# Kernel tuning notes

Hardware: AMD Instinct MI355X
Metric: run time of the kernel (lower is better)

Reference implementation:

```python
import jax, jax.numpy as jnp
import numpy as np

BLOCK = 64
# NF4 codebook (normal-float 4-bit values, as in QLoRA/torchao)
NF4_TABLE = jnp.array([
    -1.0, -0.6961928009986877, -0.5250730514526367, -0.39491748809814453,
    -0.28444138169288635, -0.18477343022823334, -0.09105003625154495, 0.0,
    0.07958029955625534, 0.16093020141124725, 0.24611230194568634,
    0.33791524171829224, 0.44070982933044434, 0.5626170039176941,
    0.7229568362236023, 1.0], dtype=jnp.float32)

D_MODEL, HIDDEN = 4096, 11008
BATCH, SEQ = 2, 2048


def setup_inputs() -> dict:
    key = jax.random.key(0)
    ks = jax.random.split(key, 7)
    x = jax.random.normal(ks[0], (BATCH, SEQ, D_MODEL), dtype=jnp.float32)
    w1_q = jax.random.randint(ks[1], (HIDDEN, D_MODEL), 0, 16, dtype=jnp.int32)
    w2_q = jax.random.randint(ks[2], (HIDDEN, D_MODEL), 0, 16, dtype=jnp.int32)
    w3_q = jax.random.randint(ks[3], (D_MODEL, HIDDEN), 0, 16, dtype=jnp.int32)
    # per-block absmax scales (positive, typical weight magnitude ~0.02)
    w1_scale = jax.random.uniform(ks[4], (HIDDEN, D_MODEL // BLOCK), dtype=jnp.float32) * 0.04
    w2_scale = jax.random.uniform(ks[5], (HIDDEN, D_MODEL // BLOCK), dtype=jnp.float32) * 0.04
    w3_scale = jax.random.uniform(ks[6], (D_MODEL, HIDDEN // BLOCK), dtype=jnp.float32) * 0.04
    return {"x": x, "w1_q": w1_q, "w1_scale": w1_scale,
            "w2_q": w2_q, "w2_scale": w2_scale,
            "w3_q": w3_q, "w3_scale": w3_scale}


def dequant_nf4(q, scale):
    # q: [O, I] int codes in [0,16); scale: [O, I//BLOCK]
    O, I = q.shape
    vals = NF4_TABLE[q]                               # lookup -> [O, I]
    vals = vals.reshape(O, I // BLOCK, BLOCK) * scale[:, :, None]
    return vals.reshape(O, I)


def reference(x, w1_q, w1_scale, w2_q, w2_scale, w3_q, w3_scale):
    w1 = dequant_nf4(w1_q, w1_scale)                  # [H, D]
    w2 = dequant_nf4(w2_q, w2_scale)                  # [H, D]
    w3 = dequant_nf4(w3_q, w3_scale)                  # [D, H]
    h = jax.nn.silu(jnp.einsum('bsd,hd->bsh', x, w1)) * jnp.einsum('bsd,hd->bsh', x, w2)
    return jnp.einsum('bsh,dh->bsd', h, w3)
```

## Files before the change

kernel.cpp:

```cpp
#include <hip/hip_runtime.h>
#include <hip/hip_bf16.h>

typedef unsigned short u16;
typedef __bf16  bf16x8 __attribute__((ext_vector_type(8)));
typedef float   f32x4  __attribute__((ext_vector_type(4)));

__device__ __constant__ float NF4C[16] = {
    -1.0f, -0.6961928009986877f, -0.5250730514526367f, -0.39491748809814453f,
    -0.28444138169288635f, -0.18477343022823334f, -0.09105003625154495f, 0.0f,
    0.07958029955625534f, 0.16093020141124725f, 0.24611230194568634f,
    0.33791524171829224f, 0.44070982933044434f, 0.5626170039176941f,
    0.7229568362236023f, 1.0f };

__device__ __forceinline__ u16 f2bf(float f) {
    union { float f; unsigned u; } v; v.f = f;
    unsigned r = v.u + 0x7FFFu + ((v.u >> 16) & 1u);
    return (u16)(r >> 16);
}
__device__ __forceinline__ float bf2f(u16 b) {
    union { unsigned u; float f; } v; v.u = ((unsigned)b) << 16;
    return v.f;
}

__device__ __forceinline__ void gl2lds16(const void* g, void* l) {
    __builtin_amdgcn_global_load_lds(
        (__attribute__((address_space(1))) void*)g,
        (__attribute__((address_space(3))) void*)l,
        16, 0, 0);
}

#define WAITVM(N)  asm volatile("s_waitcnt vmcnt(" #N ")" ::: "memory")
#define SCHED0()   __builtin_amdgcn_sched_barrier(0)
#define BAR()      __builtin_amdgcn_s_barrier()

__global__ __launch_bounds__(256) void cast_f32_bf16(
    const float* __restrict__ in, u16* __restrict__ out, int n8) {
    int i = blockIdx.x * 256 + threadIdx.x;
    if (i >= n8) return;
    const float4* p = (const float4*)in + (size_t)i * 2;
    float4 a = p[0], b = p[1];
    union { u16 u[8]; uint4 v; } r;
    r.u[0] = f2bf(a.x); r.u[1] = f2bf(a.y); r.u[2] = f2bf(a.z); r.u[3] = f2bf(a.w);
    r.u[4] = f2bf(b.x); r.u[5] = f2bf(b.y); r.u[6] = f2bf(b.z); r.u[7] = f2bf(b.w);
    ((uint4*)out)[i] = r.v;
}

__global__ __launch_bounds__(256) void dequant_nf4(
    const int* __restrict__ q, const float* __restrict__ s,
    u16* __restrict__ w, int I, int spr) {
    __shared__ float tab[16];
    if (threadIdx.x < 16) tab[threadIdx.x] = NF4C[threadIdx.x];
    __syncthreads();
    int col = (blockIdx.x * 256 + threadIdx.x) * 8;
    if (col >= I) return;
    int row = blockIdx.y;
    size_t base = (size_t)row * I + col;
    int4 c0 = *(const int4*)(q + base);
    int4 c1 = *(const int4*)(q + base + 4);
    float sc = s[(size_t)row * spr + (col >> 6)];
    union { u16 u[8]; uint4 v; } r;
    r.u[0] = f2bf(tab[c0.x & 15] * sc);
    r.u[1] = f2bf(tab[c0.y & 15] * sc);
    r.u[2] = f2bf(tab[c0.z & 15] * sc);
    r.u[3] = f2bf(tab[c0.w & 15] * sc);
    r.u[4] = f2bf(tab[c1.x & 15] * sc);
    r.u[5] = f2bf(tab[c1.y & 15] * sc);
    r.u[6] = f2bf(tab[c1.z & 15] * sc);
    r.u[7] = f2bf(tab[c1.w & 15] * sc);
    *(uint4*)(w + base) = r.v;
}

template<int EPI>
__global__ __launch_bounds__(512, 2) void gemm_bt(
    const u16* __restrict__ A, const u16* __restrict__ B,
    void* Cout, const u16* gate, int K, int ldc) {
    __shared__ u16 lA[2 * 16384];
    __shared__ u16 lB[2 * 16384];

    const int tid  = threadIdx.x;
    const int lane = tid & 63;
    const int wv   = tid >> 6;

    const int NT = gridDim.x, MT = gridDim.y;
    int id  = blockIdx.y * NT + blockIdx.x;
    int nid = (id & 7) * ((NT * MT) >> 3) + (id >> 3);
    const int bx = nid / MT;
    const int by = nid - bx * MT;

    const int sr = lane >> 2;
    const int sq = (lane & 3) ^ ((sr >> 1) & 3);

    const int gA0 = ((wv & 4) << 1) + (wv & 3);
    const int gA1 = gA0 + 4;
    const int gB0 = ((wv >> 1) << 2) + (wv & 1);
    const int gB1 = gB0 + 2;

    const u16* pA0 = A + (size_t)(by * 256 + gA0 * 16 + sr) * K + (sq << 3);
    const u16* pA1 = A + (size_t)(by * 256 + gA1 * 16 + sr) * K + (sq << 3);
    const u16* pB0 = B + (size_t)(bx * 256 + gB0 * 16 + sr) * K + (sq << 3);
    const u16* pB1 = B + (size_t)(bx * 256 + gB1 * 16 + sr) * K + (sq << 3);

    const int sA0 = gA0 * 512 + lane * 8;
    const int sA1 = gA1 * 512 + lane * 8;
    const int sB0 = gB0 * 512 + lane * 8;
    const int sB1 = gB1 * 512 + lane * 8;

    const int r16    = lane & 15;
    const int pq     = lane >> 4;
    const int slot16 = (r16 << 2) + (pq ^ ((r16 >> 1) & 3));
    const int aBase  = ((wv & 1) << 12) + slot16 * 8;
    const int bBase  = ((wv >> 1) << 11) + slot16 * 8;

#define STG_A0(TT, D) do { const u16* g_ = pA0 + (size_t)(TT) * 64;       \
        u16* l_ = lA + ((D) << 14) + sA0;                                 \
        gl2lds16(g_, l_); gl2lds16(g_ + 32, l_ + 8192); } while (0)
#define STG_A1(TT, D) do { const u16* g_ = pA1 + (size_t)(TT) * 64;       \
        u16* l_ = lA + ((D) << 14) + sA1;                                 \
        gl2lds16(g_, l_); gl2lds16(g_ + 32, l_ + 8192); } while (0)
#define STG_B0(TT, D) do { const u16* g_ = pB0 + (size_t)(TT) * 64;       \
        u16* l_ = lB + ((D) << 14) + sB0;                                 \
        gl2lds16(g_, l_); gl2lds16(g_ + 32, l_ + 8192); } while (0)
#define STG_B1(TT, D) do { const u16* g_ = pB1 + (size_t)(TT) * 64;       \
        u16* l_ = lB + ((D) << 14) + sB1;                                 \
        gl2lds16(g_, l_); gl2lds16(g_ + 32, l_ + 8192); } while (0)

#define DSR_A(C_, QM) do {                                                \
        const u16* b_ = lA + ((C_) << 14) + aBase + (QM) * (4 * 512);     \
        _Pragma("unroll")                                                 \
        for (int mm = 0; mm < 4; ++mm) {                                  \
            af[mm * 2 + 0] = *(const bf16x8*)(b_ + mm * 512);             \
            af[mm * 2 + 1] = *(const bf16x8*)(b_ + mm * 512 + 8192);      \
        } } while (0)
#define DSR_B(C_, QN) do {                                                \
        const u16* b_ = lB + ((C_) << 14) + bBase + (QN) * (2 * 512);     \
        _Pragma("unroll")                                                 \
        for (int jj = 0; jj < 2; ++jj) {                                  \
            bf[(QN) * 4 + jj * 2 + 0] = *(const bf16x8*)(b_ + jj * 512);  \
            bf[(QN) * 4 + jj * 2 + 1] = *(const bf16x8*)(b_ + jj * 512 + 8192); \
        } } while (0)

#define MFMA_Q(QM, QN) do {                                               \
        _Pragma("unroll")                                                 \
        for (int kk = 0; kk < 2; ++kk)                                    \
        _Pragma("unroll")                                                 \
        for (int mm = 0; mm < 4; ++mm)                                    \
        _Pragma("unroll")                                                 \
        for (int jj = 0; jj < 2; ++jj)                                    \
            acc[(QM) * 4 + mm][(QN) * 2 + jj] =                           \
                __builtin_amdgcn_mfma_f32_16x16x32_bf16(                  \
                    af[mm * 2 + kk], bf[(QN) * 4 + jj * 2 + kk],          \
                    acc[(QM) * 4 + mm][(QN) * 2 + jj], 0, 0, 0);          \
    } while (0)

#define KTILE(T_, C_, O_) do {                                            \
        const int t1_ = ((T_) + 1 < KT) ? (T_) + 1 : KT - 1;              \
        const int t2_ = ((T_) + 2 < KT) ? (T_) + 2 : KT - 1;              \
                                          \
        DSR_A(C_, 0); DSR_B(C_, 0); DSR_B(C_, 1);                         \
        STG_A1(t1_, O_); STG_B1(t1_, O_);                                 \
        SCHED0(); BAR(); SCHED0();                                        \
        __builtin_amdgcn_s_setprio(1);                                    \
        MFMA_Q(0, 0); MFMA_Q(0, 1);                                       \
        __builtin_amdgcn_s_setprio(0);                                    \
        SCHED0(); BAR(); SCHED0();                                        \
                                          \
        DSR_A(C_, 1);                                                     \
        STG_A0(t2_, C_); STG_B0(t2_, C_);                                 \
        WAITVM(4);                                                        \
        SCHED0(); BAR(); SCHED0();                                        \
        __builtin_amdgcn_s_setprio(1);                                    \
        MFMA_Q(1, 0); MFMA_Q(1, 1);                                       \
        __builtin_amdgcn_s_setprio(0);                                    \
        SCHED0(); BAR(); SCHED0();                                        \
    } while (0)

    f32x4 acc[8][4] = {};
    bf16x8 af[8], bf[8];
    const int KT = K >> 6;

    STG_A0(0, 0); STG_B0(0, 0); STG_A1(0, 0); STG_B1(0, 0);
    STG_A0(1, 1); STG_B0(1, 1);
    WAITVM(4);
    BAR(); SCHED0();

    for (int T = 0; T < KT; T += 2) {
        KTILE(T, 0, 1);
        KTILE(T + 1, 1, 0);
    }

    const int en   = lane & 15;
    const int er   = (lane >> 4) << 2;
    const int row0 = by * 256 + ((wv & 1) << 7);
    const int col0 = bx * 256 + ((wv >> 1) << 6);
    #pragma unroll
    for (int i = 0; i < 8; ++i) {
        int rowb = row0 + i * 16 + er;
        #pragma unroll
        for (int j = 0; j < 4; ++j) {
            int col = col0 + j * 16 + en;
            #pragma unroll
            for (int r = 0; r < 4; ++r) {
                size_t idx = (size_t)(rowb + r) * ldc + col;
                float v = acc[i][j][r];
                if (EPI == 0) {
                    ((u16*)Cout)[idx] = f2bf(v);
                } else if (EPI == 1) {
                    float g = bf2f(gate[idx]);
                    float sg = g / (1.0f + __expf(-g));
                    ((u16*)Cout)[idx] = f2bf(sg * v);
                } else {
                    ((float*)Cout)[idx] = v;
                }
            }
        }
    }
#undef STG_A0
#undef STG_A1
#undef STG_B0
#undef STG_B1
#undef DSR_A
#undef DSR_B
#undef MFMA_Q
#undef KTILE
}

extern "C" void kernel_launch(void* const* d_in, const int* in_sizes, int n_in,
                              void* d_out, int out_size, void* d_ws, size_t ws_size,
                              hipStream_t stream) {
    const float* x   = (const float*)d_in[0];
    const int*   w1q = (const int*)d_in[1];
    const float* w1s = (const float*)d_in[2];
    const int*   w2q = (const int*)d_in[3];
    const float* w2s = (const float*)d_in[4];
    const int*   w3q = (const int*)d_in[5];
    const float* w3s = (const float*)d_in[6];
    float* out = (float*)d_out;

    const int M = 4096, D = 4096, H = 11008;

    u16* xb = (u16*)d_ws;
    u16* wb = xb + (size_t)M * D;
    u16* hb = wb + (size_t)H * D;

    cast_f32_bf16<<<(M * D / 8 + 255) / 256, 256, 0, stream>>>(x, xb, M * D / 8);

    dim3 dqg1((D / 8 + 255) / 256, H);
    dequant_nf4<<<dqg1, 256, 0, stream>>>(w1q, w1s, wb, D, D / 64);
    gemm_bt<0><<<dim3(H / 256, M / 256), 512, 0, stream>>>(xb, wb, hb, nullptr, D, H);

    dequant_nf4<<<dqg1, 256, 0, stream>>>(w2q, w2s, wb, D, D / 64);
    gemm_bt<1><<<dim3(H / 256, M / 256), 512, 0, stream>>>(xb, wb, hb, hb, D, H);

    dim3 dqg3((H / 8 + 255) / 256, D);
    dequant_nf4<<<dqg3, 256, 0, stream>>>(w3q, w3s, wb, H, H / 64);
    gemm_bt<2><<<dim3(D / 256, M / 256), 512, 0, stream>>>(hb, wb, out, nullptr, H, D);
}
```

Before: 1.713 ms.

## Replace split half-tile pipeline with simple double-buffered k-tile loop

Restructures the GEMM main loop from a four-barrier schedule that staged half tiles two steps ahead into a simpler double buffer. Each iteration issues all global-to-LDS loads for the next tile, reads the full B fragment and A by k-slice from LDS, runs the MFMAs, then waits for all loads and does one barrier. This cuts the barrier count per tile and simplifies the schedule. In exchange, prefetch depth drops to one tile and each iteration ends with a full vmcnt(0) wait, so global load latency may be exposed more.

```diff
diff --git a/kernel.cpp b/kernel.cpp
--- a/kernel.cpp
+++ b/kernel.cpp
@@ -124,63 +124,53 @@
         u16* l_ = lB + ((D) << 14) + sB1;                                 \
         gl2lds16(g_, l_); gl2lds16(g_ + 32, l_ + 8192); } while (0)
 
-#define DSR_A(C_, QM) do {                                                \
-        const u16* b_ = lA + ((C_) << 14) + aBase + (QM) * (4 * 512);     \
-        _Pragma("unroll")                                                 \
-        for (int mm = 0; mm < 4; ++mm) {                                  \
-            af[mm * 2 + 0] = *(const bf16x8*)(b_ + mm * 512);             \
-            af[mm * 2 + 1] = *(const bf16x8*)(b_ + mm * 512 + 8192);      \
+#define DSR_A_K(C_, KS) do {                                              \
+        const u16* b_ = lA + ((C_) << 14) + aBase + (KS) * 8192;          \
+        _Pragma("unroll")                                                 \
+        for (int mm = 0; mm < 8; ++mm)                                    \
+            af[mm] = *(const bf16x8*)(b_ + mm * 512);                     \
+    } while (0)
+#define DSR_B_ALL(C_) do {                                                \
+        const u16* b_ = lB + ((C_) << 14) + bBase;                        \
+        _Pragma("unroll")                                                 \
+        for (int jj = 0; jj < 4; ++jj) {                                  \
+            bf[jj * 2 + 0] = *(const bf16x8*)(b_ + jj * 512);             \
+            bf[jj * 2 + 1] = *(const bf16x8*)(b_ + jj * 512 + 8192);      \
         } } while (0)
-#define DSR_B(C_, QN) do {                                                \
-        const u16* b_ = lB + ((C_) << 14) + bBase + (QN) * (2 * 512);     \
-        _Pragma("unroll")                                                 \
-        for (int jj = 0; jj < 2; ++jj) {                                  \
-            bf[(QN) * 4 + jj * 2 + 0] = *(const bf16x8*)(b_ + jj * 512);  \
-            bf[(QN) * 4 + jj * 2 + 1] = *(const bf16x8*)(b_ + jj * 512 + 8192); \
-        } } while (0)
-
-#define MFMA_Q(QM, QN) do {                                               \
-        _Pragma("unroll")                                                 \
-        for (int kk = 0; kk < 2; ++kk)                                    \
-        _Pragma("unroll")                                                 \
-        for (int mm = 0; mm < 4; ++mm)                                    \
-        _Pragma("unroll")                                                 \
-        for (int jj = 0; jj < 2; ++jj)                                    \
-            acc[(QM) * 4 + mm][(QN) * 2 + jj] =                           \
-                __builtin_amdgcn_mfma_f32_16x16x32_bf16(                  \
-                    af[mm * 2 + kk], bf[(QN) * 4 + jj * 2 + kk],          \
-                    acc[(QM) * 4 + mm][(QN) * 2 + jj], 0, 0, 0);          \
+
+#define MFMA_K(KS) do {                                                   \
+        __builtin_amdgcn_s_setprio(1);                                    \
+        _Pragma("unroll")                                                 \
+        for (int mm = 0; mm < 8; ++mm)                                    \
+        _Pragma("unroll")                                                 \
+        for (int jj = 0; jj < 4; ++jj)                                    \
+            acc[mm][jj] = __builtin_amdgcn_mfma_f32_16x16x32_bf16(        \
+                af[mm], bf[jj * 2 + (KS)], acc[mm][jj], 0, 0, 0);         \
+        __builtin_amdgcn_s_setprio(0);                                    \
     } while (0)
 
 #define KTILE(T_, C_, O_) do {                                            \
         const int t1_ = ((T_) + 1 < KT) ? (T_) + 1 : KT - 1;              \
-        const int t2_ = ((T_) + 2 < KT) ? (T_) + 2 : KT - 1;              \
-                                          \
-        DSR_A(C_, 0); DSR_B(C_, 0); DSR_B(C_, 1);                         \
-        STG_A1(t1_, O_); STG_B1(t1_, O_);                                 \
-        SCHED0(); BAR(); SCHED0();                                        \
-        __builtin_amdgcn_s_setprio(1);                                    \
-        MFMA_Q(0, 0); MFMA_Q(0, 1);                                       \
-        __builtin_amdgcn_s_setprio(0);                                    \
-        SCHED0(); BAR(); SCHED0();                                        \
-                                          \
-        DSR_A(C_, 1);                                                     \
-        STG_A0(t2_, C_); STG_B0(t2_, C_);                                 \
-        WAITVM(4);                                                        \
-        SCHED0(); BAR(); SCHED0();                                        \
-        __builtin_amdgcn_s_setprio(1);                                    \
-        MFMA_Q(1, 0); MFMA_Q(1, 1);                                       \
-        __builtin_amdgcn_s_setprio(0);                                    \
-        SCHED0(); BAR(); SCHED0();                                        \
+        STG_A0(t1_, O_); STG_A1(t1_, O_);                                 \
+        STG_B0(t1_, O_); STG_B1(t1_, O_);                                 \
+        SCHED0();                                                         \
+        DSR_B_ALL(C_);                                                    \
+        DSR_A_K(C_, 0);                                                   \
+        MFMA_K(0);                                                        \
+        DSR_A_K(C_, 1);                                                   \
+        MFMA_K(1);                                                        \
+        SCHED0();                                                         \
+        WAITVM(0);                                                        \
+        BAR();                                                            \
+        SCHED0();                                                         \
     } while (0)
 
     f32x4 acc[8][4] = {};
     bf16x8 af[8], bf[8];
     const int KT = K >> 6;
 
-    STG_A0(0, 0); STG_B0(0, 0); STG_A1(0, 0); STG_B1(0, 0);
-    STG_A0(1, 1); STG_B0(1, 1);
-    WAITVM(4);
+    STG_A0(0, 0); STG_A1(0, 0); STG_B0(0, 0); STG_B1(0, 0);
+    WAITVM(0);
     BAR(); SCHED0();
 
     for (int T = 0; T < KT; T += 2) {
@@ -218,9 +208,9 @@
 #undef STG_A1
 #undef STG_B0
 #undef STG_B1
-#undef DSR_A
-#undef DSR_B
-#undef MFMA_Q
+#undef DSR_A_K
+#undef DSR_B_ALL
+#undef MFMA_K
 #undef KTILE
 }
 
```

Result: no change. 1.716 ms (+0.2%).
